# Kernel optimization log

Measured on AMD Instinct MI355X. Metric: run time of the kernel, lower is better.

The kernel has to match this reference:

```python
import jax, jax.numpy as jnp
import numpy as np

L, B, H, P = 2048, 32, 128, 256  # seq len, batch, feature dim, state dim


def setup_inputs() -> dict:
    key = jax.random.key(0)
    ks = jax.random.split(key, 9)
    log_min, log_max = np.log(0.001), np.log(0.1)
    return {
        "input_sequences": jax.random.normal(ks[0], (L, B, H), dtype=jnp.float32),
        # -Lambda.real of a HiPPO block diag is positive; emulate with small positive values
        "log_Lambda_real": jnp.log(0.5 + jax.random.uniform(ks[1], (P,), dtype=jnp.float32)),
        "Lambda_imag": jax.random.normal(ks[2], (P,), dtype=jnp.float32) * 3.0,
        "B_tilde_r": jax.random.normal(ks[3], (P, H), dtype=jnp.float32) * (0.5 / np.sqrt(H)),
        "B_tilde_i": jax.random.normal(ks[4], (P, H), dtype=jnp.float32) * (0.5 / np.sqrt(H)),
        "C_tilde_r": jax.random.normal(ks[5], (H, P), dtype=jnp.float32) * (0.5 / np.sqrt(P)),
        "C_tilde_i": jax.random.normal(ks[6], (H, P), dtype=jnp.float32) * (0.5 / np.sqrt(P)),
        "D": jax.random.normal(ks[7], (H,), dtype=jnp.float32),
        "log_Delta": log_min + (log_max - log_min) * jax.random.uniform(ks[8], (P,), dtype=jnp.float32),
    }


def reference(input_sequences, log_Lambda_real, Lambda_imag, B_tilde_r, B_tilde_i,
              C_tilde_r, C_tilde_i, D, log_Delta):
    l = input_sequences.shape[0]
    u = input_sequences.astype(jnp.complex64)  # (L,B,H)
    lam = (-jnp.exp(log_Lambda_real) + 1j * Lambda_imag).astype(jnp.complex64)  # (P,)
    log_Lambda_bar = lam * jnp.exp(log_Delta).astype(jnp.complex64)  # scale_factor=1.0
    # kernel[t, p] = exp(log_Lambda_bar[p] * (L-1-t))  -> (L,P)
    steps = jnp.arange(l - 1, -1, -1, dtype=jnp.float32).astype(jnp.complex64)
    kernel = jnp.exp(steps[:, None] * log_Lambda_bar[None, :])
    B_tilde = (B_tilde_r + 1j * B_tilde_i).astype(jnp.complex64)  # (P,H)
    B_bar = ((kernel[-2] - 1.0) / lam)[:, None] * B_tilde  # (P,H)
    Bu = jnp.einsum('nm,lbm->lbn', B_bar, u)  # (L,B,P)
    # FFT convolution: flipped kernel is exp(log_Lambda_bar * t)
    kff = jnp.fft.fft(kernel[::-1], n=2 * l, axis=0)[:, None, :]  # (2L,1,P)
    buff = jnp.fft.fft(Bu, n=2 * l, axis=0)  # (2L,B,P)
    o = jnp.fft.ifft(kff * buff, axis=0)[:l]  # (L,B,P)
    xs = jnp.einsum('hn,lbn->lbh', (C_tilde_r + 1j * C_tilde_i).astype(jnp.complex64), o)
    xs = xs + (D * input_sequences).astype(jnp.complex64)
    return jnp.real(xs)
```

## Files before the change

### kernel.cpp

```cpp
#include <hip/hip_runtime.h>
#include <math.h>

#define SL 2048
#define NB 32
#define NH 128
#define NP 256
#define NP2 512

typedef short bf16x8 __attribute__((ext_vector_type(8)));
typedef float f32x4  __attribute__((ext_vector_type(4)));

static __device__ __forceinline__ unsigned short f2bf(float x) {
    unsigned u = __float_as_uint(x);
    return (unsigned short)((u + 0x7fffu + ((u >> 16) & 1u)) >> 16);
}
static __device__ __forceinline__ float bf2f(unsigned short h) {
    return __uint_as_float(((unsigned)h) << 16);
}
static __device__ __forceinline__ void discretize(
    const float* __restrict__ logLr, const float* __restrict__ Lim,
    const float* __restrict__ logDt, int p, float& wr, float& wi)
{
    const float Lr = expf(logLr[p]);
    const float dt = expf(logDt[p]);
    const float ew = expf(-Lr * dt);
    const float ang = Lim[p] * dt;
    wr = ew * cosf(ang); wi = ew * sinf(ang);
}

__global__ __launch_bounds__(256) void k0(
    const float* __restrict__ logLr, const float* __restrict__ Lim,
    const float* __restrict__ logDt,
    const float* __restrict__ Br, const float* __restrict__ Bi,
    const float* __restrict__ Cr, const float* __restrict__ Ci,
    unsigned short* __restrict__ Bhat, unsigned short* __restrict__ ChatF)
{
    const int tid = blockIdx.x * 256 + threadIdx.x;
    const int p = tid >> 7, h = tid & 127;
    float wr, wi; discretize(logLr, Lim, logDt, p, wr, wi);
    const float Lr = expf(logLr[p]), li = Lim[p];
    const float nr = wr - 1.0f, ni = wi;
    const float den = Lr * Lr + li * li;
    const float fr = (-nr * Lr + ni * li) / den;
    const float fi = (-ni * Lr - nr * li) / den;
    const float br = Br[p * NH + h], bi = Bi[p * NH + h];
    Bhat[(size_t)(2 * p)     * NH + h] = f2bf(fr * br - fi * bi);
    Bhat[(size_t)(2 * p + 1) * NH + h] = f2bf(fr * bi + fi * br);
    const int col0 = 2 * p, col1 = 2 * p + 1;
    ChatF[((size_t)(col0 >> 5) << 12) + (h << 5) + (col0 & 31)] = f2bf(Cr[h * NP + p]);
    ChatF[((size_t)(col1 >> 5) << 12) + (h << 5) + (col1 & 31)] = f2bf(-Ci[h * NP + p]);
}

__global__ __launch_bounds__(256, 2) void gA(
    const float* __restrict__ u, const unsigned short* __restrict__ Bhat,
    const float* __restrict__ logLr, const float* __restrict__ Lim,
    const float* __restrict__ logDt,
    unsigned short* __restrict__ bu, float2* __restrict__ part)
{
    __shared__ unsigned short us[32][136];
    __shared__ unsigned xs[32 * 257];

    const int seg = blockIdx.x;
    const int b   = blockIdx.y;
    const int tid = threadIdx.x;
    const int wave = tid >> 6, lane = tid & 63;
    const int q = lane >> 4, c = lane & 15;
    const int pbase = wave * 128;

    bf16x8 A[4][8];
    #pragma unroll
    for (int kk = 0; kk < 4; ++kk)
        #pragma unroll
        for (int mt = 0; mt < 8; ++mt)
            A[kk][mt] = *(const bf16x8*)(Bhat + (size_t)(pbase + 16 * mt + c) * NH
                                              + kk * 32 + 8 * q);

    float wr, wi; discretize(logLr, Lim, logDt, tid, wr, wi);

    for (int t = 0; t < 4; ++t) {
        const int l0 = seg * 128 + t * 32;
        __syncthreads();
        {
            const int lrow = tid >> 3;
            const int hcol = (tid & 7) * 16;
            const float* up = u + (size_t)(l0 + lrow) * (NB * NH) + b * NH + hcol;
            float4 a = *(const float4*)(up + 0);
            float4 d = *(const float4*)(up + 4);
            float4 e = *(const float4*)(up + 8);
            float4 g = *(const float4*)(up + 12);
            uint4 w0, w1;
            w0.x = (unsigned)f2bf(a.x) | ((unsigned)f2bf(a.y) << 16);
            w0.y = (unsigned)f2bf(a.z) | ((unsigned)f2bf(a.w) << 16);
            w0.z = (unsigned)f2bf(d.x) | ((unsigned)f2bf(d.y) << 16);
            w0.w = (unsigned)f2bf(d.z) | ((unsigned)f2bf(d.w) << 16);
            w1.x = (unsigned)f2bf(e.x) | ((unsigned)f2bf(e.y) << 16);
            w1.y = (unsigned)f2bf(e.z) | ((unsigned)f2bf(e.w) << 16);
            w1.z = (unsigned)f2bf(g.x) | ((unsigned)f2bf(g.y) << 16);
            w1.w = (unsigned)f2bf(g.z) | ((unsigned)f2bf(g.w) << 16);
            *(uint4*)&us[lrow][hcol + 0] = w0;
            *(uint4*)&us[lrow][hcol + 8] = w1;
        }
        __syncthreads();

        f32x4 acc[8][2];
        #pragma unroll
        for (int mt = 0; mt < 8; ++mt)
            #pragma unroll
            for (int nt = 0; nt < 2; ++nt) acc[mt][nt] = (f32x4){0.f, 0.f, 0.f, 0.f};

        #pragma unroll
        for (int kk = 0; kk < 4; ++kk) {
            bf16x8 bfr[2];
            #pragma unroll
            for (int nt = 0; nt < 2; ++nt)
                bfr[nt] = *(const bf16x8*)&us[16 * nt + c][kk * 32 + 8 * q];
            #pragma unroll
            for (int mt = 0; mt < 8; ++mt)
                #pragma unroll
                for (int nt = 0; nt < 2; ++nt)
                    acc[mt][nt] = __builtin_amdgcn_mfma_f32_16x16x32_bf16(
                        A[kk][mt], bfr[nt], acc[mt][nt], 0, 0, 0);
        }

        #pragma unroll
        for (int mt = 0; mt < 8; ++mt)
            #pragma unroll
            for (int nt = 0; nt < 2; ++nt) {
                const int rw = 16 * nt + c;
                const int pp = pbase + 16 * mt + 4 * q;
                ushort4 st;
                st.x = f2bf(acc[mt][nt][0]); st.y = f2bf(acc[mt][nt][1]);
                st.z = f2bf(acc[mt][nt][2]); st.w = f2bf(acc[mt][nt][3]);
                *(ushort4*)(bu + ((size_t)(b * SL + l0 + rw)) * NP2 + pp) = st;
                const int col = (pp >> 1);
                xs[rw * 257 + col]     = (unsigned)st.x | ((unsigned)st.y << 16);
                xs[rw * 257 + col + 1] = (unsigned)st.z | ((unsigned)st.w << 16);
            }
        __syncthreads();

        {
            float sr = 0.f, si = 0.f;
            unsigned va[8], vb[8];
            #pragma unroll
            for (int j = 0; j < 8; ++j) va[j] = xs[j * 257 + tid];
            #pragma unroll
            for (int k8 = 0; k8 < 4; ++k8) {
                if (k8 < 3) {
                    #pragma unroll
                    for (int j = 0; j < 8; ++j) vb[j] = xs[((k8 + 1) * 8 + j) * 257 + tid];
                }
                #pragma unroll
                for (int j = 0; j < 8; ++j) {
                    const float xr = bf2f((unsigned short)(va[j] & 0xffffu));
                    const float xi = bf2f((unsigned short)(va[j] >> 16));
                    const float tr = wr * sr - wi * si + xr;
                    const float ti = wr * si + wi * sr + xi;
                    sr = tr; si = ti;
                }
                #pragma unroll
                for (int j = 0; j < 8; ++j) va[j] = vb[j];
            }
            part[((size_t)b * 64 + seg * 4 + t) * NP + tid] = make_float2(sr, si);
        }
    }
}

__global__ __launch_bounds__(256) void s2(
    float2* __restrict__ part, const float* __restrict__ logLr,
    const float* __restrict__ Lim, const float* __restrict__ logDt)
{
    const int b = blockIdx.x, p = threadIdx.x;
    float wr, wi; discretize(logLr, Lim, logDt, p, wr, wi);
    float Wr = wr, Wi = wi;
    #pragma unroll
    for (int t = 0; t < 5; ++t) { const float r = Wr * Wr - Wi * Wi; Wi = 2.f * Wr * Wi; Wr = r; }
    const size_t base = (size_t)b * 64 * NP + p;
    float sr = 0.f, si = 0.f;
    float2 va[8], vb[8];
    #pragma unroll
    for (int j = 0; j < 8; ++j) va[j] = part[base + (size_t)j * NP];
    #pragma unroll
    for (int k8 = 0; k8 < 8; ++k8) {
        if (k8 < 7) {
            #pragma unroll
            for (int j = 0; j < 8; ++j)
                vb[j] = part[base + (size_t)((k8 + 1) * 8 + j) * NP];
        }
        #pragma unroll
        for (int j = 0; j < 8; ++j) {
            part[base + (size_t)(k8 * 8 + j) * NP] = make_float2(sr, si);
            const float tr = Wr * sr - Wi * si + va[j].x;
            const float ti = Wr * si + Wi * sr + va[j].y;
            sr = tr; si = ti;
        }
        #pragma unroll
        for (int j = 0; j < 8; ++j) va[j] = vb[j];
    }
}

__global__ __launch_bounds__(256, 4) void gB(
    const unsigned* __restrict__ bu32, const unsigned short* __restrict__ ChatF,
    const float* __restrict__ logLr, const float* __restrict__ Lim,
    const float* __restrict__ logDt, const float2* __restrict__ Ent,
    const float* __restrict__ Dv, const float* __restrict__ u,
    float* __restrict__ out)
{
    __shared__ char   osb[16384];
    __shared__ float2 carr[3 * 128];

    const int m = blockIdx.x, b = blockIdx.y;
    const int tid = threadIdx.x;
    const int w = tid >> 6, lane = tid & 63;
    const int q = lane >> 4, c = lane & 15;
    const int hbase = w * 32;
    const int lbase = m * 32;

    f32x4 acc[2][2];
    #pragma unroll
    for (int mt = 0; mt < 2; ++mt)
        #pragma unroll
        for (int nt = 0; nt < 2; ++nt) acc[mt][nt] = (f32x4){0.f, 0.f, 0.f, 0.f};

    #pragma unroll 1
    for (int half = 0; half < 2; ++half) {
        const int pc0 = half * 128 + lane * 2;

        float wr[2], wi[2];
        #pragma unroll
        for (int e = 0; e < 2; ++e) discretize(logLr, Lim, logDt, pc0 + e, wr[e], wi[e]);

        float Wr[2], Wi[2];
        #pragma unroll
        for (int e = 0; e < 2; ++e) { Wr[e] = wr[e]; Wi[e] = wi[e]; }
        #pragma unroll
        for (int t = 0; t < 3; ++t)
            #pragma unroll
            for (int e = 0; e < 2; ++e) {
                const float r = Wr[e] * Wr[e] - Wi[e] * Wi[e];
                Wi[e] = 2.f * Wr[e] * Wi[e]; Wr[e] = r;
            }

        const unsigned* base = bu32 + ((size_t)(b * SL + m * 32 + w * 8)) * NP
                                    + half * 128 + lane * 2;
        uint2 va[8];
        #pragma unroll
        for (int k = 0; k < 8; ++k) va[k] = *(const uint2*)(base + (size_t)k * NP);

        float sr[2] = {0.f, 0.f}, si[2] = {0.f, 0.f};
        #pragma unroll
        for (int k = 0; k < 8; ++k) {
            unsigned vv[2] = { va[k].x, va[k].y };
            #pragma unroll
            for (int e = 0; e < 2; ++e) {
                const float xr = bf2f((unsigned short)(vv[e] & 0xffffu));
                const float xi = bf2f((unsigned short)(vv[e] >> 16));
                const float tr = wr[e] * sr[e] - wi[e] * si[e] + xr;
                const float ti = wr[e] * si[e] + wi[e] * sr[e] + xi;
                sr[e] = tr; si[e] = ti;
            }
        }
        if (w < 3) {
            #pragma unroll
            for (int e = 0; e < 2; ++e)
                carr[w * 128 + lane * 2 + e] = make_float2(sr[e], si[e]);
        }

        float Er[2], Ei[2];
        #pragma unroll
        for (int e = 0; e < 2; ++e) {
            const float2 E = Ent[((size_t)(b * 64 + m)) * NP + pc0 + e];
            Er[e] = E.x; Ei[e] = E.y;
        }

        __syncthreads();

        #pragma unroll
        for (int j = 0; j < 3; ++j) if (j < w)
            #pragma unroll
            for (int e = 0; e < 2; ++e) {
                const float2 v = carr[j * 128 + lane * 2 + e];
                const float tr = Wr[e] * Er[e] - Wi[e] * Ei[e] + v.x;
                const float ti = Wr[e] * Ei[e] + Wi[e] * Er[e] + v.y;
                Er[e] = tr; Ei[e] = ti;
            }

        #pragma unroll
        for (int e = 0; e < 2; ++e) { sr[e] = Er[e]; si[e] = Ei[e]; }
        #pragma unroll
        for (int k = 0; k < 8; ++k) {
            unsigned vv[2] = { va[k].x, va[k].y };
            unsigned ov[2];
            #pragma unroll
            for (int e = 0; e < 2; ++e) {
                const float xr = bf2f((unsigned short)(vv[e] & 0xffffu));
                const float xi = bf2f((unsigned short)(vv[e] >> 16));
                const float tr = wr[e] * sr[e] - wi[e] * si[e] + xr;
                const float ti = wr[e] * si[e] + wi[e] * sr[e] + xi;
                sr[e] = tr; si[e] = ti;
                ov[e] = (unsigned)f2bf(tr) | ((unsigned)f2bf(ti) << 16);
            }
            const int row = w * 8 + k;
            const unsigned byte = (((unsigned)row << 9) + ((unsigned)lane << 3))
                                  ^ (((unsigned)(row & 7)) << 4);
            uint2 st = { ov[0], ov[1] };
            *(uint2*)(osb + byte) = st;
        }
        __syncthreads();

        #pragma unroll 4
        for (int kl = 0; kl < 8; ++kl) {
            const int kk = half * 8 + kl;
            bf16x8 af[2];
            #pragma unroll
            for (int mt = 0; mt < 2; ++mt)
                af[mt] = *(const bf16x8*)(ChatF + ((size_t)kk << 12)
                                          + ((hbase + (mt << 4) + c) << 5) + (q << 3));
            bf16x8 bfr[2];
            #pragma unroll
            for (int nt = 0; nt < 2; ++nt) {
                const int r = 16 * nt + c;
                const unsigned byte = (((unsigned)r << 9) + ((unsigned)kl << 6)
                                       + ((unsigned)q << 4))
                                      ^ (((unsigned)(c & 7)) << 4);
                bfr[nt] = *(const bf16x8*)(osb + byte);
            }
            #pragma unroll
            for (int mt = 0; mt < 2; ++mt)
                #pragma unroll
                for (int nt = 0; nt < 2; ++nt)
                    acc[mt][nt] = __builtin_amdgcn_mfma_f32_16x16x32_bf16(
                        af[mt], bfr[nt], acc[mt][nt], 0, 0, 0);
        }
        if (half == 0) __syncthreads();
    }

    #pragma unroll
    for (int mt = 0; mt < 2; ++mt) {
        const int h4 = hbase + 16 * mt + 4 * q;
        const float4 dd = *(const float4*)(Dv + h4);
        #pragma unroll
        for (int nt = 0; nt < 2; ++nt) {
            const int l = lbase + 16 * nt + c;
            const size_t off = ((size_t)l * NB + b) * NH + h4;
            const float4 uu = *(const float4*)(u + off);
            float4 ov;
            ov.x = acc[mt][nt][0] + dd.x * uu.x;
            ov.y = acc[mt][nt][1] + dd.y * uu.y;
            ov.z = acc[mt][nt][2] + dd.z * uu.z;
            ov.w = acc[mt][nt][3] + dd.w * uu.w;
            *(float4*)(out + off) = ov;
        }
    }
}

extern "C" void kernel_launch(void* const* d_in, const int* in_sizes, int n_in,
                              void* d_out, int out_size, void* d_ws, size_t ws_size,
                              hipStream_t stream)
{
    const float* u     = (const float*)d_in[0];
    const float* logLr = (const float*)d_in[1];
    const float* Lim   = (const float*)d_in[2];
    const float* Btr   = (const float*)d_in[3];
    const float* Bti   = (const float*)d_in[4];
    const float* Ctr   = (const float*)d_in[5];
    const float* Cti   = (const float*)d_in[6];
    const float* Dv    = (const float*)d_in[7];
    const float* logDt = (const float*)d_in[8];
    float* out = (float*)d_out;

    char* ws = (char*)d_ws;
    unsigned short* bu   = (unsigned short*)ws;
    float2*         part = (float2*)(ws + 67108864);
    unsigned short* Bhat = (unsigned short*)(ws + 71303168);
    unsigned short* Chat = (unsigned short*)(ws + 71434240);

    k0<<<dim3((NP * NH) / 256), 256, 0, stream>>>(logLr, Lim, logDt,
                                                  Btr, Bti, Ctr, Cti, Bhat, Chat);
    gA<<<dim3(16, NB), 256, 0, stream>>>(u, Bhat, logLr, Lim, logDt, bu, part);
    s2<<<dim3(NB), 256, 0, stream>>>(part, logLr, Lim, logDt);
    gB<<<dim3(SL / 32, NB), 256, 0, stream>>>((const unsigned*)bu, Chat, logLr, Lim,
                                              logDt, part, Dv, u, out);
}
```

Baseline: 182.9 us.

## Split gA across state halves and time chunks for more blocks

The B-projection/chunk-scan kernel now launches one block per 32-step chunk and per half of the state dimension (64x2x32 blocks) instead of 16x32 blocks looping over four chunks. The B matrix is re-laid out in k0 into a 32-column-tiled form and loaded per k-step from global memory rather than held entirely in registers. Register and shared-memory use per block drop, so launch bounds rise to four blocks per SIMD. The aim is better occupancy and more parallel work, at the cost of re-reading B and u per block and leaving half the threads idle in the scan phase.

After: 176.8 us. 1.03x faster.

```diff
diff --git a/kernel.cpp b/kernel.cpp
--- a/kernel.cpp
+++ b/kernel.cpp
@@ -33,7 +33,7 @@
     const float* __restrict__ logDt,
     const float* __restrict__ Br, const float* __restrict__ Bi,
     const float* __restrict__ Cr, const float* __restrict__ Ci,
-    unsigned short* __restrict__ Bhat, unsigned short* __restrict__ ChatF)
+    unsigned short* __restrict__ BhatF, unsigned short* __restrict__ ChatF)
 {
     const int tid = blockIdx.x * 256 + threadIdx.x;
     const int p = tid >> 7, h = tid & 127;
@@ -44,124 +44,119 @@
     const float fr = (-nr * Lr + ni * li) / den;
     const float fi = (-ni * Lr - nr * li) / den;
     const float br = Br[p * NH + h], bi = Bi[p * NH + h];
-    Bhat[(size_t)(2 * p)     * NH + h] = f2bf(fr * br - fi * bi);
-    Bhat[(size_t)(2 * p + 1) * NH + h] = f2bf(fr * bi + fi * br);
+    BhatF[((size_t)(h >> 5) << 14) + ((2 * p)     << 5) + (h & 31)] = f2bf(fr * br - fi * bi);
+    BhatF[((size_t)(h >> 5) << 14) + ((2 * p + 1) << 5) + (h & 31)] = f2bf(fr * bi + fi * br);
     const int col0 = 2 * p, col1 = 2 * p + 1;
     ChatF[((size_t)(col0 >> 5) << 12) + (h << 5) + (col0 & 31)] = f2bf(Cr[h * NP + p]);
     ChatF[((size_t)(col1 >> 5) << 12) + (h << 5) + (col1 & 31)] = f2bf(-Ci[h * NP + p]);
 }
 
-__global__ __launch_bounds__(256, 2) void gA(
-    const float* __restrict__ u, const unsigned short* __restrict__ Bhat,
+__global__ __launch_bounds__(256, 4) void gA(
+    const float* __restrict__ u, const unsigned short* __restrict__ BhatF,
     const float* __restrict__ logLr, const float* __restrict__ Lim,
     const float* __restrict__ logDt,
     unsigned short* __restrict__ bu, float2* __restrict__ part)
 {
     __shared__ unsigned short us[32][136];
-    __shared__ unsigned xs[32 * 257];
-
-    const int seg = blockIdx.x;
-    const int b   = blockIdx.y;
+    __shared__ unsigned xs[32 * 129];
+
+    const int m  = blockIdx.x;
+    const int ph = blockIdx.y;
+    const int b  = blockIdx.z;
     const int tid = threadIdx.x;
-    const int wave = tid >> 6, lane = tid & 63;
+    const int w = tid >> 6, lane = tid & 63;
     const int q = lane >> 4, c = lane & 15;
-    const int pbase = wave * 128;
-
-    bf16x8 A[4][8];
-    #pragma unroll
-    for (int kk = 0; kk < 4; ++kk)
-        #pragma unroll
-        for (int mt = 0; mt < 8; ++mt)
-            A[kk][mt] = *(const bf16x8*)(Bhat + (size_t)(pbase + 16 * mt + c) * NH
-                                              + kk * 32 + 8 * q);
-
-    float wr, wi; discretize(logLr, Lim, logDt, tid, wr, wi);
-
-    for (int t = 0; t < 4; ++t) {
-        const int l0 = seg * 128 + t * 32;
-        __syncthreads();
-        {
-            const int lrow = tid >> 3;
-            const int hcol = (tid & 7) * 16;
-            const float* up = u + (size_t)(l0 + lrow) * (NB * NH) + b * NH + hcol;
-            float4 a = *(const float4*)(up + 0);
-            float4 d = *(const float4*)(up + 4);
-            float4 e = *(const float4*)(up + 8);
-            float4 g = *(const float4*)(up + 12);
-            uint4 w0, w1;
-            w0.x = (unsigned)f2bf(a.x) | ((unsigned)f2bf(a.y) << 16);
-            w0.y = (unsigned)f2bf(a.z) | ((unsigned)f2bf(a.w) << 16);
-            w0.z = (unsigned)f2bf(d.x) | ((unsigned)f2bf(d.y) << 16);
-            w0.w = (unsigned)f2bf(d.z) | ((unsigned)f2bf(d.w) << 16);
-            w1.x = (unsigned)f2bf(e.x) | ((unsigned)f2bf(e.y) << 16);
-            w1.y = (unsigned)f2bf(e.z) | ((unsigned)f2bf(e.w) << 16);
-            w1.z = (unsigned)f2bf(g.x) | ((unsigned)f2bf(g.y) << 16);
-            w1.w = (unsigned)f2bf(g.z) | ((unsigned)f2bf(g.w) << 16);
-            *(uint4*)&us[lrow][hcol + 0] = w0;
-            *(uint4*)&us[lrow][hcol + 8] = w1;
-        }
-        __syncthreads();
-
-        f32x4 acc[8][2];
-        #pragma unroll
-        for (int mt = 0; mt < 8; ++mt)
-            #pragma unroll
-            for (int nt = 0; nt < 2; ++nt) acc[mt][nt] = (f32x4){0.f, 0.f, 0.f, 0.f};
-
-        #pragma unroll
-        for (int kk = 0; kk < 4; ++kk) {
-            bf16x8 bfr[2];
+    const int pbase = ph * 256 + w * 64;
+    const int l0 = m * 32;
+
+    {
+        const int lrow = tid >> 3;
+        const int hcol = (tid & 7) * 16;
+        const float* up = u + (size_t)(l0 + lrow) * (NB * NH) + b * NH + hcol;
+        float4 a = *(const float4*)(up + 0);
+        float4 d = *(const float4*)(up + 4);
+        float4 e = *(const float4*)(up + 8);
+        float4 g = *(const float4*)(up + 12);
+        uint4 w0, w1;
+        w0.x = (unsigned)f2bf(a.x) | ((unsigned)f2bf(a.y) << 16);
+        w0.y = (unsigned)f2bf(a.z) | ((unsigned)f2bf(a.w) << 16);
+        w0.z = (unsigned)f2bf(d.x) | ((unsigned)f2bf(d.y) << 16);
+        w0.w = (unsigned)f2bf(d.z) | ((unsigned)f2bf(d.w) << 16);
+        w1.x = (unsigned)f2bf(e.x) | ((unsigned)f2bf(e.y) << 16);
+        w1.y = (unsigned)f2bf(e.z) | ((unsigned)f2bf(e.w) << 16);
+        w1.z = (unsigned)f2bf(g.x) | ((unsigned)f2bf(g.y) << 16);
+        w1.w = (unsigned)f2bf(g.z) | ((unsigned)f2bf(g.w) << 16);
+        *(uint4*)&us[lrow][hcol + 0] = w0;
+        *(uint4*)&us[lrow][hcol + 8] = w1;
+    }
+    __syncthreads();
+
+    f32x4 acc[4][2];
+    #pragma unroll
+    for (int mt = 0; mt < 4; ++mt)
+        #pragma unroll
+        for (int nt = 0; nt < 2; ++nt) acc[mt][nt] = (f32x4){0.f, 0.f, 0.f, 0.f};
+
+    #pragma unroll
+    for (int kk = 0; kk < 4; ++kk) {
+        bf16x8 af[4];
+        #pragma unroll
+        for (int mt = 0; mt < 4; ++mt)
+            af[mt] = *(const bf16x8*)(BhatF + ((size_t)kk << 14)
+                                      + ((pbase + 16 * mt + c) << 5) + 8 * q);
+        bf16x8 bfr[2];
+        #pragma unroll
+        for (int nt = 0; nt < 2; ++nt)
+            bfr[nt] = *(const bf16x8*)&us[16 * nt + c][kk * 32 + 8 * q];
+        #pragma unroll
+        for (int mt = 0; mt < 4; ++mt)
             #pragma unroll
             for (int nt = 0; nt < 2; ++nt)
-                bfr[nt] = *(const bf16x8*)&us[16 * nt + c][kk * 32 + 8 * q];
-            #pragma unroll
-            for (int mt = 0; mt < 8; ++mt)
+                acc[mt][nt] = __builtin_amdgcn_mfma_f32_16x16x32_bf16(
+                    af[mt], bfr[nt], acc[mt][nt], 0, 0, 0);
+    }
+
+    #pragma unroll
+    for (int mt = 0; mt < 4; ++mt)
+        #pragma unroll
+        for (int nt = 0; nt < 2; ++nt) {
+            const int rw  = 16 * nt + c;
+            const int ppl = w * 64 + 16 * mt + 4 * q;
+            const int pp  = ph * 256 + ppl;
+            ushort4 st;
+            st.x = f2bf(acc[mt][nt][0]); st.y = f2bf(acc[mt][nt][1]);
+            st.z = f2bf(acc[mt][nt][2]); st.w = f2bf(acc[mt][nt][3]);
+            *(ushort4*)(bu + ((size_t)(b * SL + l0 + rw)) * NP2 + pp) = st;
+            const int col = (ppl >> 1);
+            xs[rw * 129 + col]     = (unsigned)st.x | ((unsigned)st.y << 16);
+            xs[rw * 129 + col + 1] = (unsigned)st.z | ((unsigned)st.w << 16);
+        }
+    __syncthreads();
+
+    if (tid < 128) {
+        float wr, wi; discretize(logLr, Lim, logDt, ph * 128 + tid, wr, wi);
+        float sr = 0.f, si = 0.f;
+        unsigned va[8], vb[8];
+        #pragma unroll
+        for (int j = 0; j < 8; ++j) va[j] = xs[j * 129 + tid];
+        #pragma unroll
+        for (int k8 = 0; k8 < 4; ++k8) {
+            if (k8 < 3) {
                 #pragma unroll
-                for (int nt = 0; nt < 2; ++nt)
-                    acc[mt][nt] = __builtin_amdgcn_mfma_f32_16x16x32_bf16(
-                        A[kk][mt], bfr[nt], acc[mt][nt], 0, 0, 0);
-        }
-
-        #pragma unroll
-        for (int mt = 0; mt < 8; ++mt)
-            #pragma unroll
-            for (int nt = 0; nt < 2; ++nt) {
-                const int rw = 16 * nt + c;
-                const int pp = pbase + 16 * mt + 4 * q;
-                ushort4 st;
-                st.x = f2bf(acc[mt][nt][0]); st.y = f2bf(acc[mt][nt][1]);
-                st.z = f2bf(acc[mt][nt][2]); st.w = f2bf(acc[mt][nt][3]);
-                *(ushort4*)(bu + ((size_t)(b * SL + l0 + rw)) * NP2 + pp) = st;
-                const int col = (pp >> 1);
-                xs[rw * 257 + col]     = (unsigned)st.x | ((unsigned)st.y << 16);
-                xs[rw * 257 + col + 1] = (unsigned)st.z | ((unsigned)st.w << 16);
-            }
-        __syncthreads();
-
-        {
-            float sr = 0.f, si = 0.f;
-            unsigned va[8], vb[8];
-            #pragma unroll
-            for (int j = 0; j < 8; ++j) va[j] = xs[j * 257 + tid];
-            #pragma unroll
-            for (int k8 = 0; k8 < 4; ++k8) {
-                if (k8 < 3) {
-                    #pragma unroll
-                    for (int j = 0; j < 8; ++j) vb[j] = xs[((k8 + 1) * 8 + j) * 257 + tid];
-                }
-                #pragma unroll
-                for (int j = 0; j < 8; ++j) {
-                    const float xr = bf2f((unsigned short)(va[j] & 0xffffu));
-                    const float xi = bf2f((unsigned short)(va[j] >> 16));
-                    const float tr = wr * sr - wi * si + xr;
-                    const float ti = wr * si + wi * sr + xi;
-                    sr = tr; si = ti;
-                }
-                #pragma unroll
-                for (int j = 0; j < 8; ++j) va[j] = vb[j];
-            }
-            part[((size_t)b * 64 + seg * 4 + t) * NP + tid] = make_float2(sr, si);
-        }
+                for (int j = 0; j < 8; ++j) vb[j] = xs[((k8 + 1) * 8 + j) * 129 + tid];
+            }
+            #pragma unroll
+            for (int j = 0; j < 8; ++j) {
+                const float xr = bf2f((unsigned short)(va[j] & 0xffffu));
+                const float xi = bf2f((unsigned short)(va[j] >> 16));
+                const float tr = wr * sr - wi * si + xr;
+                const float ti = wr * si + wi * sr + xi;
+                sr = tr; si = ti;
+            }
+            #pragma unroll
+            for (int j = 0; j < 8; ++j) va[j] = vb[j];
+        }
+        part[((size_t)b * 64 + m) * NP + ph * 128 + tid] = make_float2(sr, si);
     }
 }
 
@@ -376,7 +371,7 @@
 
     k0<<<dim3((NP * NH) / 256), 256, 0, stream>>>(logLr, Lim, logDt,
                                                   Btr, Bti, Ctr, Cti, Bhat, Chat);
-    gA<<<dim3(16, NB), 256, 0, stream>>>(u, Bhat, logLr, Lim, logDt, bu, part);
+    gA<<<dim3(SL / 32, 2, NB), 256, 0, stream>>>(u, Bhat, logLr, Lim, logDt, bu, part);
     s2<<<dim3(NB), 256, 0, stream>>>(part, logLr, Lim, logDt);
     gB<<<dim3(SL / 32, NB), 256, 0, stream>>>((const unsigned*)bu, Chat, logLr, Lim,
                                               logDt, part, Dv, u, out);
```
